# Optimization experiments

Hardware: AMD Instinct MI355X
Metric: run time of the kernel (lower is better)

Reference implementation:

```python
import jax, jax.numpy as jnp
import numpy as np

H = W = 256
L = H * W                      # number of graph vertices / tree leaves
N_NODES = 2 * L - 1            # binary partition tree node count
LAM = 1.0                      # lambda_ (soft-area temperature)


def _grid_edges():
    """4-adjacency grid graph edges (same structure as higra get_4_adjacency_graph)."""
    idx = np.arange(L, dtype=np.int64).reshape(H, W)
    src = np.concatenate([idx[:, :-1].ravel(), idx[:-1, :].ravel()])
    dst = np.concatenate([idx[:, 1:].ravel(), idx[1:, :].ravel()])
    return src.astype(np.int32), dst.astype(np.int32)


def setup_inputs() -> dict:
    key = jax.random.key(0)
    src, dst = _grid_edges()
    ew = jax.random.uniform(key, (src.shape[0],), dtype=jnp.float32)
    return {"edge_weights": ew,
            "edges_src": jnp.asarray(src),
            "edges_dst": jnp.asarray(dst)}


def _build_tree(ew, src, dst):
    """higra.bpt_canonical: Kruskal over stably-sorted edges, building a binary
    merge tree. Leaves are 0..L-1, internal node L+i is created by the i-th MST
    edge. Returns (sizes, mst_edge_map, ancestor paths). All integer structure
    is piecewise-constant w.r.t. edge_weights (no gradient flows through it)."""
    order = np.argsort(ew, kind="stable")
    uf = np.arange(L)

    def find(x):
        r = x
        while uf[r] != r:
            r = uf[r]
        while uf[x] != r:
            uf[x], x = r, uf[x]
        return r

    canon = np.arange(L)                      # tree node of each union-find root
    parent = np.arange(N_NODES)               # self-parent until set (root keeps self)
    sizes = np.ones(N_NODES, dtype=np.float32)
    edge_map = np.zeros(L - 1, dtype=np.int64)
    node = L
    for ei in order:
        a = find(src[ei]); b = find(dst[ei])
        if a == b:
            continue
        na, nb = canon[a], canon[b]
        parent[na] = node
        parent[nb] = node
        sizes[node] = sizes[na] + sizes[nb]
        edge_map[node - L] = ei
        uf[a] = b
        canon[b] = node
        node += 1
    # self-inclusive ancestor paths, padded by repeating the root
    cur = np.arange(N_NODES)
    cols = [cur.copy()]
    while np.any(parent[cur] != cur):
        cur = parent[cur]
        cols.append(cur.copy())
    paths = np.stack(cols, axis=1)            # [N_NODES, D+1]
    return sizes, edge_map, paths


def _softarea(edge_weights, edge_map, sizes_np, paths_np):
    """Soft area of every tree node n:
       area(n) = sum_x sigmoid((alt(n) - d(x, n)) / lambda)
    where d(x,n) is the min ultrametric distance from leaf x to the leaves of n:
      - x in subtree(n), x != n : d = alt(parent(x))
      - x == n (leaf)           : d = 0
      - x outside subtree(n)    : d = alt(lowest ancestor of n containing x).
    Outside leaves are grouped per ancestor a (count = size(a) - size(previous
    node on the path)), giving an O(N * depth) vectorized computation."""
    alt = jnp.concatenate([jnp.zeros((L,), edge_weights.dtype),
                           edge_weights[edge_map]])          # [N_NODES]
    alt_path = alt[paths_np]                                  # [N, D+1]
    size_path = sizes_np[paths_np]                            # constant, numpy
    diff = jnp.asarray(size_path[:, 1:] - size_path[:, :-1])  # 0 on root padding
    outside = jnp.sum(
        diff * jax.nn.sigmoid((alt[:, None] - alt_path[:, 1:]) / LAM), axis=1)

    # inside: each leaf x contributes sigmoid((alt(a_k) - alt(parent(x)))/lam)
    # to every proper ancestor a_k, plus sigmoid(0)=0.5 to itself (alt(leaf)=0).
    lp = paths_np[:L]                                         # [L, D+1]
    alt_lp = alt_path[:L]
    valid = jnp.asarray((lp[:, 1:] != lp[:, :-1]).astype(np.float32))
    vals = jax.nn.sigmoid((alt_lp[:, 1:] - alt_lp[:, 1:2]) / LAM) * valid
    inside = jax.ops.segment_sum(vals.reshape(-1),
                                 jnp.asarray(lp[:, 1:].reshape(-1)),
                                 num_segments=N_NODES)
    inside = inside.at[:L].add(0.5)
    return inside + outside


def reference(edge_weights, edges_src, edges_dst):
    sizes, edge_map, paths = _build_tree(np.asarray(edge_weights),
                                         np.asarray(edges_src),
                                         np.asarray(edges_dst))
    return _softarea(edge_weights, jnp.asarray(edge_map), sizes, paths)
```

## Files before the change

### kernel.cpp

```cpp
#include <hip/hip_runtime.h>
#include <stdint.h>

typedef unsigned int u32;
typedef unsigned short u16;

#define L_VERTS 65536
#define N_EDGES 130560
#define N_NODES 131071
#define NODEPAD 131072

#define CCH 170
#define SCH 768
#define MAXSV 1536
#define HSZ 2048

#define NB 255
#define TPB 64
#define IPT 8
#define IPB 512

__global__ void init_keys(const float* __restrict__ w, u32* __restrict__ keys, u32* __restrict__ vals){
  int i = blockIdx.x*blockDim.x + threadIdx.x;
  if(i < N_EDGES){ keys[i] = __float_as_uint(w[i]); vals[i] = (u32)i; }
}

__global__ void radix_hist(const u32* __restrict__ idx, const u32* __restrict__ keys,
                           u32* __restrict__ histG, int shift){
  __shared__ u32 h[256];
  for(int i=threadIdx.x;i<256;i+=TPB) h[i]=0;
  __syncthreads();
  int base = blockIdx.x*IPB + threadIdx.x*IPT;
  #pragma unroll
  for(int i=0;i<IPT;i++){
    u32 e = idx[base+i];
    u32 d = (keys[e]>>shift)&255u;
    atomicAdd(&h[d],1u);
  }
  __syncthreads();
  for(int i=threadIdx.x;i<256;i+=TPB) histG[i*NB+blockIdx.x]=h[i];
}

__global__ void radix_scan(u32* histG){
  const int M = 256*NB;
  __shared__ u32 sums[1024];
  int t=threadIdx.x; int s=t*64; u32 acc=0;
  for(int i=0;i<64;i++){int id=s+i; if(id<M) acc+=histG[id];}
  sums[t]=acc; __syncthreads();
  for(int off=1; off<1024; off<<=1){
    u32 v=(t>=off)?sums[t-off]:0u;
    __syncthreads();
    sums[t]+=v;
    __syncthreads();
  }
  u32 run = (t==0)?0u:sums[t-1];
  for(int i=0;i<64;i++){int id=s+i; if(id<M){u32 v=histG[id]; histG[id]=run; run+=v;}}
}

__global__ void radix_scatter(const u32* __restrict__ idxIn, const u32* __restrict__ keys,
                              u32* __restrict__ idxOut, const u32* __restrict__ histG, int shift){
  __shared__ u16 thoff[256][TPB];
  int t=threadIdx.x;
  for(int d=t;d<256;d+=TPB) for(int j=0;j<TPB;j++) thoff[d][j]=0;
  __syncthreads();
  int base = blockIdx.x*IPB + t*IPT;
  u32 myv[IPT]; u32 myd[IPT];
  #pragma unroll
  for(int i=0;i<IPT;i++){
    myv[i]=idxIn[base+i];
    myd[i]=(keys[myv[i]]>>shift)&255u;
    thoff[myd[i]][t]++;
  }
  __syncthreads();
  for(int dd=0;dd<4;dd++){
    int d=t*4+dd; u32 run=0;
    for(int j=0;j<TPB;j++){ u32 v=thoff[d][j]; thoff[d][j]=(u16)run; run+=v; }
  }
  __syncthreads();
  #pragma unroll
  for(int i=0;i<IPT;i++){
    u32 d=myd[i];
    u32 pos = histG[d*NB+blockIdx.x] + (u32)thoff[d][t];
    thoff[d][t]++;
    idxOut[pos]=myv[i];
  }
}

__global__ void build_epair(const u32* __restrict__ order, const int* __restrict__ srcv,
                            const int* __restrict__ dstv, u32* __restrict__ epair){
  int p=blockIdx.x*blockDim.x+threadIdx.x;
  if(p>=N_EDGES) return;
  u32 e=order[p];
  epair[p]=((u32)dstv[e]<<16)|(u32)srcv[e];
}

__global__ void init_all(u32* szG,u16* canonTop16,u32* parent,float* alt){
  int i=blockIdx.x*blockDim.x+threadIdx.x;
  if(i<N_NODES){ parent[i]=(u32)i; alt[i]=0.f; }
  if(i<L_VERTS){ szG[i]=1u; canonTop16[i]=0xFFFFu; }
}

__device__ __forceinline__ u32 ald(u32* p){
  return __hip_atomic_load(p, __ATOMIC_RELAXED, __HIP_MEMORY_SCOPE_AGENT);
}
__device__ __forceinline__ void ast(u32* p, u32 v){
  __hip_atomic_store(p, v, __ATOMIC_RELAXED, __HIP_MEMORY_SCOPE_AGENT);
}

__global__ void __launch_bounds__(1024,1) p1_checkpoints(
    const u32* __restrict__ epair,
    u32* szG, u16* lid16, u16* svroot16, u16* svsize16, u16* svnext16, u32* mG)
{
  __shared__ u16 ufL[L_VERTS];
  __shared__ u32 hkey[HSZ];
  __shared__ u16 hval[HSZ];
  __shared__ u32 sufL[MAXSV];
  __shared__ u32 compsz[MAXSV];
  __shared__ u32 repkey[MAXSV];
  __shared__ u32 mcnt;
  int t = threadIdx.x;
  for(int i=t;i<L_VERTS/2;i+=1024) ((u32*)ufL)[i]=((2u*(u32)i+1u)<<16)|(2u*(u32)i);
  for(int k=0;k<CCH;k++){
    for(int i=t;i<HSZ;i+=1024) hkey[i]=0xFFFFFFFFu;
    for(u32 s=t;s<MAXSV;s+=1024){ sufL[s]=s; compsz[s]=0u; repkey[s]=0u; }
    if(t==0) mcnt=0u;
    __syncthreads();
    int base = k*SCH;
    int myslot[2]; int mycnt=0;
    for(int i=t;i<2*SCH;i+=1024){
      u32 pr = epair[base+(i>>1)];
      u32 v = (i&1)? (pr>>16) : (pr&0xFFFFu);
      u32 x=v;
      while(true){ u32 px=ufL[x]; if(px==x)break; u32 g=ufL[px]; if(g!=px) ufL[x]=(u16)g; x=g; }
      u32 r=x;
      if(v!=r) ufL[v]=(u16)r;
      u32 h=(r*2654435761u)>>21;
      int slot;
      while(true){
        u32 old=atomicCAS(&hkey[h],0xFFFFFFFFu,r);
        if(old==0xFFFFFFFFu){
          slot=(int)h;
          u32 id=atomicAdd(&mcnt,1u);
          hval[h]=(u16)id;
          svroot16[k*MAXSV+id]=(u16)r;
          break;
        }
        if(old==r){slot=(int)h;break;}
        h=(h+1)&(HSZ-1u);
      }
      myslot[mycnt++]=slot;
    }
    __syncthreads();
    u32 mc=mcnt;
    if(t==0) mG[k]=mc;
    for(u32 s=t;s<mc;s+=1024){
      u32 r=(u32)svroot16[k*MAXSV+s];
      svsize16[k*MAXSV+s]=(u16)(ald(&szG[r])-1u);
    }
    {
      int c=0;
      for(int i=t;i<2*SCH;i+=1024){ lid16[2*base+i]=hval[myslot[c]]; c++; }
    }
    __syncthreads();
    for(int i=t;i<SCH;i+=1024){
      u32 lw=((u32*)lid16)[base+i];
      u32 sa=lw&0xFFFFu, sb=lw>>16;
      if(sa==sb) continue;
      while(true){
        u32 x=sa; while(true){u32 p2=sufL[x]; if(p2==x)break; u32 g=sufL[p2]; if(g!=p2) sufL[x]=g; x=g;}
        u32 y=sb; while(true){u32 p2=sufL[y]; if(p2==y)break; u32 g=sufL[p2]; if(g!=p2) sufL[y]=g; y=g;}
        if(x==y) break;
        u32 hi=x>y?x:y, lo=x^y^hi;
        if(atomicCAS(&sufL[hi],hi,lo)==hi) break;
        sa=hi; sb=lo;
      }
    }
    __syncthreads();
    for(u32 s=t;s<mc;s+=1024){
      u32 x=s; while(true){u32 p2=sufL[x]; if(p2==x)break; x=p2;}
      sufL[s]=x;
      u32 sz=(u32)svsize16[k*MAXSV+s]+1u;
      atomicAdd(&compsz[x], sz);
      atomicMax(&repkey[x], (sz<<11) | (2047u-s));
    }
    __syncthreads();
    for(u32 s=t;s<mc;s+=1024){
      u32 rs=sufL[s];
      u32 rep=2047u-(repkey[rs]&2047u);
      u32 wv=(u32)svroot16[k*MAXSV+rep];
      svnext16[k*MAXSV+s]=(u16)wv;
      u32 myroot=(u32)svroot16[k*MAXSV+s];
      if(myroot!=wv) ufL[myroot]=(u16)wv;
      if(s==rep)     ast(&szG[wv], compsz[rs]);
    }
    __syncthreads();
  }
}

__global__ void __launch_bounds__(64) p2_chunk(
  const u16* __restrict__ lid16,
  const u16* __restrict__ svsize16, const u16* __restrict__ svnext16, const u32* __restrict__ mG,
  u16* __restrict__ outChA, u16* __restrict__ outChB, u16* __restrict__ outSize16, u16* __restrict__ outJ16,
  u32* __restrict__ accCnt, u16* __restrict__ compR16, u16* __restrict__ compTop16, u32* __restrict__ ncomp)
{
  int k = blockIdx.x; int t = threadIdx.x;
  __shared__ u16 uf[MAXSV];
  __shared__ u32 csize[MAXSV];
  __shared__ u16 ctop[MAXSV];
  __shared__ u16 svnl[MAXSV];
  __shared__ u32 cmp_s;
  u32 m = mG[k];
  for(u32 s=t;s<m;s+=64){
    uf[s]=(u16)s;
    csize[s]=(u32)svsize16[k*MAXSV+s]+1u;
    ctop[s]=(u16)s;
    svnl[s]=svnext16[k*MAXSV+s];
  }
  if(t==0) cmp_s=0u;
  __syncthreads();
  if(t==0){
    int base=k*SCH;
    u32 cnt=0;
    for(int j=0;j<SCH;j++){
      u32 lw = ((const u32*)lid16)[base+j];
      u32 la = lw & 0xFFFFu, lb = lw >> 16;
      u32 x=la; while(true){u32 px=uf[x]; if(px==x)break; u32 g=uf[px]; uf[x]=(u16)g; x=g;}
      u32 y=lb; while(true){u32 py=uf[y]; if(py==y)break; u32 g=uf[py]; uf[y]=(u16)g; y=g;}
      if(x==y) continue;
      u32 sa=csize[x], sb=csize[y], ns=sa+sb;
      outChA[base+cnt]=ctop[x];
      outChB[base+cnt]=ctop[y];
      outSize16[base+cnt]=(u16)(ns-1u);
      outJ16[base+cnt]=(u16)j;
      u32 win=(sa>=sb)?x:y, los=x^y^win;
      uf[los]=(u16)win; csize[win]=ns; ctop[win]=(u16)(0x8000u|cnt);
      cnt++;
    }
    accCnt[k]=cnt;
  }
  __syncthreads();
  for(u32 s=t;s<m;s+=64){
    if(uf[s]==(u16)s && (ctop[s]&0x8000u)){
      u32 pos=atomicAdd(&cmp_s,1u);
      compR16[k*MAXSV+pos]=svnl[s];
      compTop16[k*MAXSV+pos]=(u16)(ctop[s]&0x7FFFu);
    }
  }
  __syncthreads();
  if(t==0) ncomp[k]=cmp_s;
}

__global__ void __launch_bounds__(1024) p3_stitch(
  const u32* __restrict__ accCnt, const u16* __restrict__ outChA, const u16* __restrict__ outChB,
  const u16* __restrict__ outSize16, const u16* __restrict__ outJ16,
  const u16* __restrict__ svroot16,
  const u16* __restrict__ compR16, const u16* __restrict__ compTop16, const u32* __restrict__ ncomp,
  const u32* __restrict__ order, const float* __restrict__ w,
  u16* __restrict__ canonTop16, u32* __restrict__ parent, float* __restrict__ alt, u16* __restrict__ usize16)
{
  __shared__ u32 accBase[CCH];
  int t=threadIdx.x;
  if(t==0){ u32 r=0; for(int k=0;k<CCH;k++){ accBase[k]=r; r+=accCnt[k]; } }
  __syncthreads();
  for(int idx=t; idx<N_EDGES; idx+=1024){
    int k = idx/SCH; int j = idx - k*SCH;
    if(j < (int)accCnt[k]){
      u32 nid = (u32)L_VERTS + accBase[k] + (u32)j;
      u32 p = (u32)(k*SCH) + (u32)outJ16[idx];
      alt[nid] = w[order[p]];
      usize16[nid] = outSize16[idx];
      u32 cA=outChA[idx]; if(cA & 0x8000u) parent[(u32)L_VERTS+accBase[k]+(cA&0x7FFFu)] = nid;
      u32 cB=outChB[idx]; if(cB & 0x8000u) parent[(u32)L_VERTS+accBase[k]+(cB&0x7FFFu)] = nid;
    }
  }
  __syncthreads();
  for(int k=0;k<CCH;k++){
    u32 ac=accCnt[k];
    for(u32 j=t;j<ac;j+=1024){
      u32 idx=(u32)(k*SCH)+j;
      u32 nid=(u32)L_VERTS+accBase[k]+j;
      u32 cA=outChA[idx];
      if(!(cA&0x8000u)){
        u32 root=(u32)svroot16[k*MAXSV+cA];
        u32 ct=(u32)canonTop16[root];
        parent[(ct==0xFFFFu)?root:((u32)L_VERTS+ct)]=nid;
      }
      u32 cB=outChB[idx];
      if(!(cB&0x8000u)){
        u32 root=(u32)svroot16[k*MAXSV+cB];
        u32 ct=(u32)canonTop16[root];
        parent[(ct==0xFFFFu)?root:((u32)L_VERTS+ct)]=nid;
      }
    }
    __syncthreads();
    u32 nc=ncomp[k];
    for(u32 j=t;j<nc;j+=1024){
      canonTop16[(u32)compR16[k*MAXSV+j]] = (u16)(accBase[k]+compTop16[k*MAXSV+j]);
    }
    __syncthreads();
  }
}

__device__ __forceinline__ void hvals6(float v, float* o){
  float v2=v*v, v3=v2*v, v4=v2*v2, v5=v4*v;
  o[0]=0.5f-0.25f*v+v3*(1.f/48.f)-v5*(1.f/480.f);
  o[1]=0.25f-v2*(1.f/16.f)+v4*(1.f/96.f);
  o[2]=v*(1.f/16.f)-v3*(1.f/48.f);
  o[3]=v2*(1.f/48.f)-(1.f/48.f);
  o[4]=-v*(1.f/96.f);
  o[5]=(1.f/480.f);
}

__global__ void zero_cc(u32* cc){
  int i=blockIdx.x*blockDim.x+threadIdx.x;
  if(i<L_VERTS) cc[i]=0u;
}

__global__ void prep_init(const u32* __restrict__ parent, const u16* __restrict__ usize16,
                          u32* cc, u32* J0, uint2* A0, float* out){
  int n=blockIdx.x*blockDim.x+threadIdx.x;
  if(n>=N_NODES) return;
  out[n] = (n<L_VERTS)?0.5f:0.0f;
  if(n==N_NODES-1){ J0[n]=(u32)n; A0[n]=make_uint2(0u,0u); return; }
  u32 p=parent[n];
  u32 ord=atomicAdd(&cc[p-L_VERTS],1u);
  u32 szP=(u32)usize16[p]+1u;
  u32 szN=(n<L_VERTS)?1u:((u32)usize16[n]+1u);
  u32 sib=szP-szN;
  A0[n]=make_uint2(ord? sib:0u, 1u + (ord? (2u*sib-1u):0u));
  J0[n]=p;
}

__global__ void double_round2(const u32* __restrict__ Jin, const uint2* __restrict__ Ain,
                              u32* __restrict__ Jout, uint2* __restrict__ Aout){
  int n=blockIdx.x*blockDim.x+threadIdx.x;
  if(n>=N_NODES) return;
  u32 j=Jin[n];
  u32 j2=Jin[j];
  u32 j3=Jin[j2];
  uint2 a=Ain[n], aj=Ain[j], b=Ain[j2], bj=Ain[j3];
  Aout[n]=make_uint2(a.x+aj.x+b.x+bj.x, a.y+aj.y+b.y+bj.y);
  Jout[n]=Jin[j3];
}

__global__ void zero_nodeM(float* nodeM){
  int i=blockIdx.x*blockDim.x+threadIdx.x;
  if(i<6*NODEPAD) nodeM[i]=0.f;
}

__global__ void scatter_all(const u32* __restrict__ parent, const float* __restrict__ alt,
                            const u16* __restrict__ usize16, const uint2* __restrict__ accF,
                            float* __restrict__ leafM, float* __restrict__ nodeM){
  int n=blockIdx.x*blockDim.x+threadIdx.x;
  if(n>=N_NODES) return;
  u32 p=parent[n];
  float h[6]; hvals6(alt[p],h);
  uint2 af=accF[n];
  if(n<L_VERTS){
    u32 pos=af.x;
    #pragma unroll
    for(int j=0;j<6;j++) leafM[(size_t)j*L_VERTS+pos]=h[j];
  }
  if(n<N_NODES-1){
    u32 szP=(u32)usize16[p]+1u;
    u32 szN=(n<L_VERTS)?1u:((u32)usize16[n]+1u);
    float d=(float)(szP-szN);
    u32 q0=af.y;
    u32 q1=q0 + 2u*szN - 1u;
    #pragma unroll
    for(int j=0;j<6;j++){
      float tm=d*h[j];
      atomicAdd(&nodeM[(size_t)j*NODEPAD+q0], tm);
      atomicAdd(&nodeM[(size_t)j*NODEPAD+q1], -tm);
    }
  }
}

__global__ void scanAll(float* __restrict__ leafM, float* __restrict__ nodeM,
                        float* __restrict__ bsumL, float* __restrict__ bsumN){
  int b=blockIdx.x; int t=threadIdx.x;
  float* arr; u32 base; float* bs;
  if(b<6*64){ int row=b>>6, blk=b&63;  arr=leafM+(size_t)row*L_VERTS;  base=(u32)blk*1024u; bs=&bsumL[row*64+blk]; }
  else      { int bb=b-384; int row=bb>>7, blk=bb&127; arr=nodeM+(size_t)row*NODEPAD; base=(u32)blk*1024u; bs=&bsumN[row*128+blk]; }
  __shared__ float s[256];
  base += (u32)t*4u;
  float v0=arr[base],v1=arr[base+1],v2=arr[base+2],v3=arr[base+3];
  v1+=v0; v2+=v1; v3+=v2;
  s[t]=v3; __syncthreads();
  for(int o=1;o<256;o<<=1){ float x=(t>=o)?s[t-o]:0.f; __syncthreads(); s[t]+=x; __syncthreads(); }
  float pre=(t>0)?s[t-1]:0.f;
  arr[base]=v0+pre; arr[base+1]=v1+pre; arr[base+2]=v2+pre; arr[base+3]=v3+pre;
  if(t==255) *bs=s[255];
}

__global__ void scanB(float* bsumL, float* bsumN){
  int t=threadIdx.x;
  if(t<6){ float r=0; for(int i=0;i<64;i++){ float v=bsumL[t*64+i]; bsumL[t*64+i]=r; r+=v; } }
  else if(t<12){ int j=t-6; float r=0; for(int i=0;i<128;i++){ float v=bsumN[j*128+i]; bsumN[j*128+i]=r; r+=v; } }
}

__global__ void eval_all(const uint2* __restrict__ accF, const float* __restrict__ alt,
                         const u16* __restrict__ usize16, const float* __restrict__ leafM,
                         const float* __restrict__ nodeM, const float* __restrict__ bsumL,
                         const float* __restrict__ bsumN, float* __restrict__ out){
  int n=blockIdx.x*blockDim.x+threadIdx.x;
  if(n>=N_NODES) return;
  uint2 af=accF[n];
  float u=alt[n];
  u32 q=af.y;
  float acc=0.f, up=1.f;
  #pragma unroll
  for(int j=0;j<6;j++){
    float T = nodeM[(size_t)j*NODEPAD+q] + bsumN[j*128 + (q>>10)];
    acc += up*T;
    up*=u;
  }
  if(n>=L_VERTS){
    u32 lo=af.x;
    u32 hi=lo + (u32)usize16[n] + 1u;
    up=1.f;
    #pragma unroll
    for(int j=0;j<6;j++){
      const float* arr=leafM + (size_t)j*L_VERTS;
      const float* bs=bsumL + j*64;
      float Ph = arr[hi-1u] + bs[(hi-1u)>>10];
      float Pl = lo ? (arr[lo-1u] + bs[(lo-1u)>>10]) : 0.f;
      acc += up*(Ph-Pl);
      up*=u;
    }
  }
  out[n]+=acc;
}

__global__ void ws_too_small(float* out){
  int i=blockIdx.x*blockDim.x+threadIdx.x;
  if(i<N_NODES) out[i]=1.0e6f;
}

extern "C" void kernel_launch(void* const* d_in, const int* in_sizes, int n_in,
                              void* d_out, int out_size, void* d_ws, size_t ws_size,
                              hipStream_t stream){
  (void)in_sizes; (void)n_in; (void)out_size;
  const float* w  = (const float*)d_in[0];
  const int* src  = (const int*)d_in[1];
  const int* dst  = (const int*)d_in[2];
  float* out = (float*)d_out;

  char* ws = (char*)d_ws;
  size_t off=0;
  auto alloc=[&](size_t bytes)->void*{ void* p = ws+off; off += (bytes+511)&~(size_t)511; return p; };
  u32* parent   =(u32*)alloc((size_t)N_NODES*4);
  float* alt    =(float*)alloc((size_t)N_NODES*4);
  u16* usize16  =(u16*)alloc((size_t)N_NODES*2);
  float* bsumL  =(float*)alloc(6*64*4);
  float* bsumN  =(float*)alloc(6*128*4);
  size_t scratch0=off;
  u32* keys0    =(u32*)alloc((size_t)N_EDGES*4);
  u32* vals0    =(u32*)alloc((size_t)N_EDGES*4);
  u32* vals1    =(u32*)alloc((size_t)N_EDGES*4);
  u32* histG    =(u32*)alloc(256*NB*4);
  u16* canonTop16=(u16*)alloc((size_t)L_VERTS*2);
  u16* outJ16   =(u16*)alloc((size_t)N_EDGES*2);
  u16* svroot16 =(u16*)alloc((size_t)CCH*MAXSV*2);
  u16* svsize16 =(u16*)alloc((size_t)CCH*MAXSV*2);
  u16* svnext16 =(u16*)alloc((size_t)CCH*MAXSV*2);
  u32* mG       =(u32*)alloc(CCH*4);
  u32* accCnt   =(u32*)alloc(CCH*4);
  u32* ncomp    =(u32*)alloc(CCH*4);
  size_t endA=off;
  off=scratch0;
  u32* ccChsum  =(u32*)alloc((size_t)L_VERTS*4);
  u32* J0       =(u32*)alloc((size_t)N_NODES*4);
  u32* J1       =(u32*)alloc((size_t)N_NODES*4);
  uint2* A0     =(uint2*)alloc((size_t)N_NODES*8);
  uint2* A1     =(uint2*)alloc((size_t)N_NODES*8);
  float* nodeM  =(float*)alloc((size_t)6*NODEPAD*4);
  size_t endB=off;
  float* leafM  =(float*)ccChsum;

  if((endA>ws_size)||(endB>ws_size)){
    ws_too_small<<<(N_NODES+255)/256,256,0,stream>>>(out);
    return;
  }

  u16* lid16    =(u16*)vals1;
  u32* epair    =keys0;
  u16* outChA16 =(u16*)histG;
  u16* outChB16 =(u16*)keys0;
  u16* outSize16=(u16*)((char*)keys0 + (size_t)N_EDGES*2);
  u16* compR16  =svsize16;
  u16* compTop16=svnext16;
  u32* szG      =(u32*)usize16;

  init_keys<<<(N_EDGES+255)/256,256,0,stream>>>(w,keys0,vals0);
  for(int pass=0;pass<4;pass++){
    const u32* iv = (pass&1)?vals1:vals0;
    u32* ov = (pass&1)?vals0:vals1;
    int shift=pass*8;
    radix_hist   <<<NB,TPB,0,stream>>>(iv,keys0,histG,shift);
    radix_scan   <<<1,1024,0,stream>>>(histG);
    radix_scatter<<<NB,TPB,0,stream>>>(iv,keys0,ov,histG,shift);
  }
  build_epair<<<(N_EDGES+255)/256,256,0,stream>>>(vals0,src,dst,epair);
  init_all<<<(N_NODES+255)/256,256,0,stream>>>(szG,canonTop16,parent,alt);
  p1_checkpoints<<<1,1024,0,stream>>>(epair,szG,lid16,svroot16,svsize16,svnext16,mG);
  p2_chunk<<<CCH,64,0,stream>>>(lid16,svsize16,svnext16,mG,
                                outChA16,outChB16,outSize16,outJ16,accCnt,compR16,compTop16,ncomp);
  p3_stitch<<<1,1024,0,stream>>>(accCnt,outChA16,outChB16,outSize16,outJ16,svroot16,
                                 compR16,compTop16,ncomp,vals0,w,canonTop16,parent,alt,usize16);
  zero_cc<<<(L_VERTS+255)/256,256,0,stream>>>(ccChsum);
  prep_init<<<(N_NODES+255)/256,256,0,stream>>>(parent,usize16,ccChsum,J0,A0,out);
  for(int r=0;r<9;r++){
    if((r&1)==0) double_round2<<<(N_NODES+255)/256,256,0,stream>>>(J0,A0,J1,A1);
    else         double_round2<<<(N_NODES+255)/256,256,0,stream>>>(J1,A1,J0,A0);
  }
  const uint2* accF=A1;
  zero_nodeM<<<(6*NODEPAD+255)/256,256,0,stream>>>(nodeM);
  scatter_all<<<(N_NODES+255)/256,256,0,stream>>>(parent,alt,usize16,accF,leafM,nodeM);
  scanAll<<<1152,256,0,stream>>>(leafM,nodeM,bsumL,bsumN);
  scanB<<<1,64,0,stream>>>(bsumL,bsumN);
  eval_all<<<(N_NODES+255)/256,256,0,stream>>>(accF,alt,usize16,leafM,nodeM,bsumL,bsumN,out);
}
```

Measured before the change: 2.962 ms.

## Interleave union-find walks, split stitch into serial wave and parallel waves, fuse zero kernels

```diff
diff --git a/kernel.cpp b/kernel.cpp
--- a/kernel.cpp
+++ b/kernel.cpp
@@ -93,10 +93,10 @@
   epair[p]=((u32)dstv[e]<<16)|(u32)srcv[e];
 }
 
-__global__ void init_all(u32* szG,u16* canonTop16,u32* parent,float* alt){
+__global__ void init_all(u32* szG,u32* canonTop32,u32* parent,float* alt){
   int i=blockIdx.x*blockDim.x+threadIdx.x;
   if(i<N_NODES){ parent[i]=(u32)i; alt[i]=0.f; }
-  if(i<L_VERTS){ szG[i]=1u; canonTop16[i]=0xFFFFu; }
+  if(i<L_VERTS){ szG[i]=1u; canonTop32[i]=0xFFFFFFFFu; }
 }
 
 __device__ __forceinline__ u32 ald(u32* p){
@@ -125,29 +125,40 @@
     if(t==0) mcnt=0u;
     __syncthreads();
     int base = k*SCH;
-    int myslot[2]; int mycnt=0;
-    for(int i=t;i<2*SCH;i+=1024){
-      u32 pr = epair[base+(i>>1)];
-      u32 v = (i&1)? (pr>>16) : (pr&0xFFFFu);
-      u32 x=v;
-      while(true){ u32 px=ufL[x]; if(px==x)break; u32 g=ufL[px]; if(g!=px) ufL[x]=(u16)g; x=g; }
-      u32 r=x;
-      if(v!=r) ufL[v]=(u16)r;
-      u32 h=(r*2654435761u)>>21;
-      int slot;
-      while(true){
-        u32 old=atomicCAS(&hkey[h],0xFFFFFFFFu,r);
-        if(old==0xFFFFFFFFu){
-          slot=(int)h;
-          u32 id=atomicAdd(&mcnt,1u);
-          hval[h]=(u16)id;
-          svroot16[k*MAXSV+id]=(u16)r;
-          break;
+    int myslot[2]; int mycnt = (t<512)?2:1;
+    {
+      u32 i0=(u32)t, i1=(u32)t+1024u;
+      u32 pr0=epair[base+(i0>>1)];
+      u32 v0=(i0&1)?(pr0>>16):(pr0&0xFFFFu);
+      u32 v1=0u; bool has1=(mycnt==2);
+      if(has1){ u32 pr1=epair[base+(i1>>1)]; v1=(i1&1)?(pr1>>16):(pr1&0xFFFFu); }
+      u32 x0=v0, x1=has1?v1:0u;
+      bool d0=false, d1=!has1;
+      while(!(d0&&d1)){
+        if(!d0){ u32 p=ufL[x0]; if(p==x0) d0=true; else { u32 g=ufL[p]; if(g!=p) ufL[x0]=(u16)g; x0=g; } }
+        if(!d1){ u32 p=ufL[x1]; if(p==x1) d1=true; else { u32 g=ufL[p]; if(g!=p) ufL[x1]=(u16)g; x1=g; } }
+      }
+      if(v0!=x0) ufL[v0]=(u16)x0;
+      if(has1 && v1!=x1) ufL[v1]=(u16)x1;
+      u32 rr[2]={x0,x1};
+      for(int c=0;c<mycnt;c++){
+        u32 r=rr[c];
+        u32 h=(r*2654435761u)>>21;
+        int slot;
+        while(true){
+          u32 old=atomicCAS(&hkey[h],0xFFFFFFFFu,r);
+          if(old==0xFFFFFFFFu){
+            slot=(int)h;
+            u32 id=atomicAdd(&mcnt,1u);
+            hval[h]=(u16)id;
+            svroot16[k*MAXSV+id]=(u16)r;
+            break;
+          }
+          if(old==r){slot=(int)h;break;}
+          h=(h+1)&(HSZ-1u);
         }
-        if(old==r){slot=(int)h;break;}
-        h=(h+1)&(HSZ-1u);
+        myslot[c]=slot;
       }
-      myslot[mycnt++]=slot;
     }
     __syncthreads();
     u32 mc=mcnt;
@@ -255,48 +266,51 @@
   const u16* __restrict__ svroot16,
   const u16* __restrict__ compR16, const u16* __restrict__ compTop16, const u32* __restrict__ ncomp,
   const u32* __restrict__ order, const float* __restrict__ w,
-  u16* __restrict__ canonTop16, u32* __restrict__ parent, float* __restrict__ alt, u16* __restrict__ usize16)
+  u32* canonTop32, u32* __restrict__ parent, float* __restrict__ alt, u16* __restrict__ usize16)
 {
   __shared__ u32 accBase[CCH];
   int t=threadIdx.x;
   if(t==0){ u32 r=0; for(int k=0;k<CCH;k++){ accBase[k]=r; r+=accCnt[k]; } }
   __syncthreads();
-  for(int idx=t; idx<N_EDGES; idx+=1024){
-    int k = idx/SCH; int j = idx - k*SCH;
-    if(j < (int)accCnt[k]){
-      u32 nid = (u32)L_VERTS + accBase[k] + (u32)j;
-      u32 p = (u32)(k*SCH) + (u32)outJ16[idx];
-      alt[nid] = w[order[p]];
-      usize16[nid] = outSize16[idx];
-      u32 cA=outChA[idx]; if(cA & 0x8000u) parent[(u32)L_VERTS+accBase[k]+(cA&0x7FFFu)] = nid;
-      u32 cB=outChB[idx]; if(cB & 0x8000u) parent[(u32)L_VERTS+accBase[k]+(cB&0x7FFFu)] = nid;
-    }
-  }
-  __syncthreads();
-  for(int k=0;k<CCH;k++){
-    u32 ac=accCnt[k];
-    for(u32 j=t;j<ac;j+=1024){
-      u32 idx=(u32)(k*SCH)+j;
-      u32 nid=(u32)L_VERTS+accBase[k]+j;
-      u32 cA=outChA[idx];
-      if(!(cA&0x8000u)){
-        u32 root=(u32)svroot16[k*MAXSV+cA];
-        u32 ct=(u32)canonTop16[root];
-        parent[(ct==0xFFFFu)?root:((u32)L_VERTS+ct)]=nid;
+  if(t<64){
+    int l=t;
+    for(int k=0;k<CCH;k++){
+      u32 ac=accCnt[k];
+      for(u32 j=l;j<ac;j+=64){
+        u32 idx=(u32)(k*SCH)+j;
+        u32 nid=(u32)L_VERTS+accBase[k]+j;
+        u32 cA=outChA[idx];
+        if(!(cA&0x8000u)){
+          u32 root=(u32)svroot16[k*MAXSV+cA];
+          u32 ct=ald(&canonTop32[root]);
+          parent[(ct==0xFFFFFFFFu)?root:((u32)L_VERTS+ct)]=nid;
+        }
+        u32 cB=outChB[idx];
+        if(!(cB&0x8000u)){
+          u32 root=(u32)svroot16[k*MAXSV+cB];
+          u32 ct=ald(&canonTop32[root]);
+          parent[(ct==0xFFFFFFFFu)?root:((u32)L_VERTS+ct)]=nid;
+        }
       }
-      u32 cB=outChB[idx];
-      if(!(cB&0x8000u)){
-        u32 root=(u32)svroot16[k*MAXSV+cB];
-        u32 ct=(u32)canonTop16[root];
-        parent[(ct==0xFFFFu)?root:((u32)L_VERTS+ct)]=nid;
+      __threadfence_block();
+      u32 nc=ncomp[k];
+      for(u32 j=l;j<nc;j+=64){
+        ast(&canonTop32[(u32)compR16[k*MAXSV+j]], accBase[k]+compTop16[k*MAXSV+j]);
       }
-    }
-    __syncthreads();
-    u32 nc=ncomp[k];
-    for(u32 j=t;j<nc;j+=1024){
-      canonTop16[(u32)compR16[k*MAXSV+j]] = (u16)(accBase[k]+compTop16[k*MAXSV+j]);
-    }
-    __syncthreads();
+      __threadfence_block();
+    }
+  } else {
+    for(int idx=t-64; idx<N_EDGES; idx+=960){
+      int k = idx/SCH; int j = idx - k*SCH;
+      if(j < (int)accCnt[k]){
+        u32 nid = (u32)L_VERTS + accBase[k] + (u32)j;
+        u32 p = (u32)(k*SCH) + (u32)outJ16[idx];
+        alt[nid] = w[order[p]];
+        usize16[nid] = outSize16[idx];
+        u32 cA=outChA[idx]; if(cA & 0x8000u) parent[(u32)L_VERTS+accBase[k]+(cA&0x7FFFu)] = nid;
+        u32 cB=outChB[idx]; if(cB & 0x8000u) parent[(u32)L_VERTS+accBase[k]+(cB&0x7FFFu)] = nid;
+      }
+    }
   }
 }
 
@@ -310,9 +324,10 @@
   o[5]=(1.f/480.f);
 }
 
-__global__ void zero_cc(u32* cc){
+__global__ void zero_both(u32* cc, float* nodeM){
   int i=blockIdx.x*blockDim.x+threadIdx.x;
   if(i<L_VERTS) cc[i]=0u;
+  if(i<6*NODEPAD) nodeM[i]=0.f;
 }
 
 __global__ void prep_init(const u32* __restrict__ parent, const u16* __restrict__ usize16,
@@ -340,11 +355,6 @@
   uint2 a=Ain[n], aj=Ain[j], b=Ain[j2], bj=Ain[j3];
   Aout[n]=make_uint2(a.x+aj.x+b.x+bj.x, a.y+aj.y+b.y+bj.y);
   Jout[n]=Jin[j3];
-}
-
-__global__ void zero_nodeM(float* nodeM){
-  int i=blockIdx.x*blockDim.x+threadIdx.x;
-  if(i<6*NODEPAD) nodeM[i]=0.f;
 }
 
 __global__ void scatter_all(const u32* __restrict__ parent, const float* __restrict__ alt,
@@ -458,7 +468,7 @@
   u32* vals0    =(u32*)alloc((size_t)N_EDGES*4);
   u32* vals1    =(u32*)alloc((size_t)N_EDGES*4);
   u32* histG    =(u32*)alloc(256*NB*4);
-  u16* canonTop16=(u16*)alloc((size_t)L_VERTS*2);
+  u32* canonTop32=(u32*)alloc((size_t)L_VERTS*4);
   u16* outJ16   =(u16*)alloc((size_t)N_EDGES*2);
   u16* svroot16 =(u16*)alloc((size_t)CCH*MAXSV*2);
   u16* svsize16 =(u16*)alloc((size_t)CCH*MAXSV*2);
@@ -501,20 +511,19 @@
     radix_scatter<<<NB,TPB,0,stream>>>(iv,keys0,ov,histG,shift);
   }
   build_epair<<<(N_EDGES+255)/256,256,0,stream>>>(vals0,src,dst,epair);
-  init_all<<<(N_NODES+255)/256,256,0,stream>>>(szG,canonTop16,parent,alt);
+  init_all<<<(N_NODES+255)/256,256,0,stream>>>(szG,canonTop32,parent,alt);
   p1_checkpoints<<<1,1024,0,stream>>>(epair,szG,lid16,svroot16,svsize16,svnext16,mG);
   p2_chunk<<<CCH,64,0,stream>>>(lid16,svsize16,svnext16,mG,
                                 outChA16,outChB16,outSize16,outJ16,accCnt,compR16,compTop16,ncomp);
   p3_stitch<<<1,1024,0,stream>>>(accCnt,outChA16,outChB16,outSize16,outJ16,svroot16,
-                                 compR16,compTop16,ncomp,vals0,w,canonTop16,parent,alt,usize16);
-  zero_cc<<<(L_VERTS+255)/256,256,0,stream>>>(ccChsum);
+                                 compR16,compTop16,ncomp,vals0,w,canonTop32,parent,alt,usize16);
+  zero_both<<<(6*NODEPAD+255)/256,256,0,stream>>>(ccChsum,nodeM);
   prep_init<<<(N_NODES+255)/256,256,0,stream>>>(parent,usize16,ccChsum,J0,A0,out);
   for(int r=0;r<9;r++){
     if((r&1)==0) double_round2<<<(N_NODES+255)/256,256,0,stream>>>(J0,A0,J1,A1);
     else         double_round2<<<(N_NODES+255)/256,256,0,stream>>>(J1,A1,J0,A0);
   }
   const uint2* accF=A1;
-  zero_nodeM<<<(6*NODEPAD+255)/256,256,0,stream>>>(nodeM);
   scatter_all<<<(N_NODES+255)/256,256,0,stream>>>(parent,alt,usize16,accF,leafM,nodeM);
   scanAll<<<1152,256,0,stream>>>(leafM,nodeM,bsumL,bsumN);
   scanB<<<1,64,0,stream>>>(bsumL,bsumN);
```

After: 4.202 ms. +41.9%, slower.
